# Performance work log

Hardware: AMD Instinct MI355X
Metric: run time of the kernel (lower is better)

The kernel has to match this reference:

```python
import jax, jax.numpy as jnp
import numpy as np

N_NODES = 50000
N_EDGES = 800000
IN_DIM = 128
OUT_DIM = 64
BN_EPS = 1e-5
LRELU_SLOPE = 0.01


def setup_inputs() -> dict:
    key = jax.random.key(0)
    ks = jax.random.split(key, 8)
    feature = jax.random.normal(ks[0], (N_NODES, IN_DIM), dtype=jnp.float32)
    src = jax.random.randint(ks[1], (N_EDGES,), 0, N_NODES)
    dst = jax.random.randint(ks[2], (N_EDGES,), 0, N_NODES)
    edge_weight = jax.random.uniform(ks[3], (N_EDGES,), dtype=jnp.float32)
    # learned params
    b1 = jnp.zeros((IN_DIM,), jnp.float32)                      # gcn1 bias (weight=False)
    gamma1 = jnp.ones((IN_DIM,), jnp.float32)
    beta1 = jnp.zeros((IN_DIM,), jnp.float32)
    W2 = jax.random.normal(ks[4], (IN_DIM, OUT_DIM), jnp.float32) * (2.0 / IN_DIM) ** 0.5  # kaiming-ish
    b2 = jnp.zeros((OUT_DIM,), jnp.float32)
    gamma2 = jnp.ones((OUT_DIM,), jnp.float32)
    beta2 = jnp.zeros((OUT_DIM,), jnp.float32)
    return dict(feature=feature, edge_weight=edge_weight, b1=b1, gamma1=gamma1,
                beta1=beta1, W2=W2, b2=b2, gamma2=gamma2, beta2=beta2,
                src=src, dst=dst)


def _degrees(src, dst, n):
    ones = jnp.ones(src.shape[0], jnp.float32)
    deg_out = jnp.clip(jax.ops.segment_sum(ones, src, num_segments=n), 1.0)
    deg_in = jnp.clip(jax.ops.segment_sum(ones, dst, num_segments=n), 1.0)
    return deg_out, deg_in


def _graph_conv(x, src, dst, edge_w, W, b, deg_out, deg_in):
    # DGL GraphConv, norm='both': D_in^{-1/2} * A(_w) * D_out^{-1/2} * x (@ W) + b
    h = x * jax.lax.rsqrt(deg_out)[:, None]
    if W is not None:
        h = h @ W  # [N, out]
    m = h[src]                                   # gather  [E, d]
    if edge_w is not None:
        m = m * edge_w[:, None]
    agg = jax.ops.segment_sum(m, dst, num_segments=x.shape[0])  # scatter-add [N, d]
    return agg * jax.lax.rsqrt(deg_in)[:, None] + b


def _batchnorm(x, gamma, beta):
    mean = jnp.mean(x, axis=0)
    var = jnp.var(x, axis=0)  # biased, as torch BN training-mode normalization
    return gamma * (x - mean) * jax.lax.rsqrt(var + BN_EPS) + beta


def reference(feature, edge_weight, b1, gamma1, beta1, W2, b2, gamma2, beta2, src, dst):
    deg_out, deg_in = _degrees(src, dst, feature.shape[0])
    h = _graph_conv(feature, src, dst, edge_weight, None, b1, deg_out, deg_in)
    h = _batchnorm(h, gamma1, beta1)              # dropout = identity (eval)
    h1 = jnp.where(h > 0, h, LRELU_SLOPE * h)     # LeakyReLU
    h2 = _graph_conv(h1, src, dst, None, W2, b2, deg_out, deg_in)
    h = _batchnorm(h2, gamma2, beta2)
    return jax.nn.softmax(h, axis=-1)
```

## Files before the change

### kernel.cpp

```cpp
#include <hip/hip_runtime.h>
#include <cstddef>

typedef unsigned int u32;

#define N_NODES 50000
#define N_EDGES 800000
#define D1 128
#define D2 64
#define BN_EPS 1e-5f
#define LRELU 0.01f
#define ELLW 64
#define C1B 2048
#define C2B 2048

__device__ __forceinline__ u32 f2bf(float x) {
    u32 u = __float_as_uint(x);
    return (u + 0x7fffu + ((u >> 16) & 1u)) >> 16;
}

__global__ void k_build(const int* __restrict__ src, const int* __restrict__ dst,
                        const float* __restrict__ ew, const float* __restrict__ feature,
                        int* __restrict__ cnt_in, int* __restrict__ cnt_out,
                        u32* __restrict__ ell, u32* __restrict__ feat_bf) {
    const int e = blockIdx.x * 256 + threadIdx.x;
    if (e < N_EDGES) {
        int d = dst[e];
        int slot = atomicAdd(&cnt_in[d], 1);
        if (slot < ELLW)
            ell[(size_t)d * ELLW + slot] = ((u32)src[e] << 16) | f2bf(ew[e]);
        atomicAdd(&cnt_out[src[e]], 1);
    }
    const int TOTU = N_NODES * (D1 / 2);
    for (int i = e; i < TOTU; i += N_EDGES) {
        float2 v = *(const float2*)&feature[2 * (size_t)i];
        feat_bf[i] = f2bf(v.x) | (f2bf(v.y) << 16);
    }
}

__global__ __launch_bounds__(128) void k_conv1(const u32* __restrict__ feat_bf,
                                               const int* __restrict__ cnt_in,
                                               const int* __restrict__ cnt_out,
                                               const u32* __restrict__ ell,
                                               const float* __restrict__ b1,
                                               float* __restrict__ t1,
                                               float* __restrict__ part1) {
    const int w = threadIdx.x >> 6, lane = threadIdx.x & 63;
    __shared__ int   s_idx[2][ELLW];
    __shared__ float s_sc[2][ELLW];
    __shared__ float red[2][D1];
    const float bb0 = b1[2 * lane], bb1 = b1[2 * lane + 1];
    float s0 = 0.f, q0 = 0.f, s1 = 0.f, q1 = 0.f;
    for (int base = blockIdx.x * 2; base < N_NODES; base += 2 * C1B) {
        const int node = base + w;
        const int cnt = cnt_in[node];
        const int deg = min(cnt, ELLW);
        if (lane < deg) {
            u32 ent = ell[(size_t)node * ELLW + lane];
            int s = ent >> 16;
            s_idx[w][lane] = s;
            s_sc[w][lane]  = __uint_as_float(ent << 16) * rsqrtf((float)max(cnt_out[s], 1));
        }
        __syncthreads();
        float a0 = 0.f, a1 = 0.f;
        for (int j = 0; j < deg; ++j) {
            u32 p = feat_bf[(size_t)s_idx[w][j] * (D1 / 2) + lane];
            float sc = s_sc[w][j];
            a0 += __uint_as_float(p << 16) * sc;
            a1 += __uint_as_float(p & 0xffff0000u) * sc;
        }
        float r = rsqrtf((float)max(cnt, 1));
        float v0 = a0 * r + bb0, v1 = a1 * r + bb1;
        float2 v = {v0, v1};
        *(float2*)&t1[(size_t)node * D1 + 2 * lane] = v;
        s0 += v0; q0 += v0 * v0; s1 += v1; q1 += v1 * v1;
        __syncthreads();
    }
    red[w][2 * lane] = s0; red[w][2 * lane + 1] = s1;
    __syncthreads();
    if (w == 0) {
        part1[(size_t)blockIdx.x * 2 * D1 + 2 * lane]     = red[0][2 * lane] + red[1][2 * lane];
        part1[(size_t)blockIdx.x * 2 * D1 + 2 * lane + 1] = red[0][2 * lane + 1] + red[1][2 * lane + 1];
    }
    __syncthreads();
    red[w][2 * lane] = q0; red[w][2 * lane + 1] = q1;
    __syncthreads();
    if (w == 0) {
        part1[(size_t)blockIdx.x * 2 * D1 + D1 + 2 * lane]     = red[0][2 * lane] + red[1][2 * lane];
        part1[(size_t)blockIdx.x * 2 * D1 + D1 + 2 * lane + 1] = red[0][2 * lane + 1] + red[1][2 * lane + 1];
    }
}

template <int D>
__global__ __launch_bounds__(128) void k_bn_final(const float* __restrict__ part, int nblk,
                                                  const float* __restrict__ gamma,
                                                  const float* __restrict__ beta,
                                                  float* __restrict__ coef) {
    const int c = blockIdx.x;
    const int t = threadIdx.x;
    __shared__ float sh[4];
    float s = 0.f, q = 0.f;
    for (int b = t; b < nblk; b += 128) {
        s += part[(size_t)b * 2 * D + c];
        q += part[(size_t)b * 2 * D + D + c];
    }
    for (int o = 32; o >= 1; o >>= 1) {
        s += __shfl_xor(s, o, 64);
        q += __shfl_xor(q, o, 64);
    }
    if ((t & 63) == 0) { sh[(t >> 6) * 2] = s; sh[(t >> 6) * 2 + 1] = q; }
    __syncthreads();
    if (t == 0) {
        s = sh[0] + sh[2];
        q = sh[1] + sh[3];
        const float inv_n = 1.f / (float)N_NODES;
        float mean = s * inv_n;
        float var  = q * inv_n - mean * mean;
        float rstd = rsqrtf(var + BN_EPS);
        float a = gamma[c] * rstd;
        coef[c]     = a;
        coef[D + c] = beta[c] - mean * a;
    }
}

__global__ __launch_bounds__(256) void k_mm(const float* __restrict__ t1,
                                            const float* __restrict__ coef1,
                                            const int* __restrict__ cnt_out,
                                            const float* __restrict__ W2,
                                            u32* __restrict__ g_bf) {
    __shared__ float sW[D1 * D2];
    __shared__ float sX[32][132];
    const int tid = threadIdx.x;
    const int r0 = blockIdx.x * 32;
    for (int i = tid; i < D1 * D2 / 4; i += 256)
        ((float4*)sW)[i] = ((const float4*)W2)[i];
    for (int i = tid; i < 32 * (D1 / 4); i += 256) {
        int r = i >> 5, k4 = i & 31;
        int row = r0 + r;
        float4 v = {0.f, 0.f, 0.f, 0.f};
        if (row < N_NODES) {
            v = *(const float4*)&t1[(size_t)row * D1 + 4 * k4];
            float ro = rsqrtf((float)max(cnt_out[row], 1));
            int k = 4 * k4;
            float x;
            x = coef1[k]     * v.x + coef1[D1 + k];     v.x = ((x > 0.f) ? x : LRELU * x) * ro;
            x = coef1[k + 1] * v.y + coef1[D1 + k + 1]; v.y = ((x > 0.f) ? x : LRELU * x) * ro;
            x = coef1[k + 2] * v.z + coef1[D1 + k + 2]; v.z = ((x > 0.f) ? x : LRELU * x) * ro;
            x = coef1[k + 3] * v.w + coef1[D1 + k + 3]; v.w = ((x > 0.f) ? x : LRELU * x) * ro;
        }
        *(float4*)&sX[r][4 * k4] = v;
    }
    __syncthreads();
    const int c  = tid & 63;
    const int rg = tid >> 6;
    float acc[8] = {0.f, 0.f, 0.f, 0.f, 0.f, 0.f, 0.f, 0.f};
    for (int k = 0; k < D1; k += 4) {
        float w0 = sW[k * D2 + c];
        float w1 = sW[(k + 1) * D2 + c];
        float w2 = sW[(k + 2) * D2 + c];
        float w3 = sW[(k + 3) * D2 + c];
#pragma unroll
        for (int j = 0; j < 8; ++j) {
            float4 x4 = *(const float4*)&sX[rg + 4 * j][k];
            acc[j] = fmaf(x4.x, w0, acc[j]);
            acc[j] = fmaf(x4.y, w1, acc[j]);
            acc[j] = fmaf(x4.z, w2, acc[j]);
            acc[j] = fmaf(x4.w, w3, acc[j]);
        }
    }
#pragma unroll
    for (int j = 0; j < 8; ++j) {
        int row = r0 + rg + 4 * j;
        float partner = __shfl_xor(acc[j], 1, 64);
        if (row < N_NODES && (c & 1) == 0)
            g_bf[(size_t)row * (D2 / 2) + (c >> 1)] = f2bf(acc[j]) | (f2bf(partner) << 16);
    }
}

__global__ __launch_bounds__(128) void k_conv2(const u32* __restrict__ g_bf,
                                               const int* __restrict__ cnt_in,
                                               const u32* __restrict__ ell,
                                               const float* __restrict__ b2,
                                               float* __restrict__ out,
                                               float* __restrict__ part2) {
    const int w = threadIdx.x >> 6, lane = threadIdx.x & 63;
    const int m = lane & 31, half = lane >> 5;
    __shared__ int   s_idx[2][ELLW];
    __shared__ float red[2][D2];
    const float bb0 = b2[2 * m], bb1 = b2[2 * m + 1];
    float s0 = 0.f, q0 = 0.f, s1 = 0.f, q1 = 0.f;
    for (int base = blockIdx.x * 2; base < N_NODES; base += 2 * C2B) {
        const int node = base + w;
        const int cnt = cnt_in[node];
        const int deg = min(cnt, ELLW);
        if (lane < deg) s_idx[w][lane] = ell[(size_t)node * ELLW + lane] >> 16;
        __syncthreads();
        float a0 = 0.f, a1 = 0.f;
        for (int j = half; j < deg; j += 2) {
            u32 p = g_bf[(size_t)s_idx[w][j] * (D2 / 2) + m];
            a0 += __uint_as_float(p << 16);
            a1 += __uint_as_float(p & 0xffff0000u);
        }
        a0 += __shfl_xor(a0, 32, 64);
        a1 += __shfl_xor(a1, 32, 64);
        float r = rsqrtf((float)max(cnt, 1));
        float v0 = a0 * r + bb0, v1 = a1 * r + bb1;
        if (half == 0) {
            float2 v = {v0, v1};
            *(float2*)&out[(size_t)node * D2 + 2 * m] = v;
            s0 += v0; q0 += v0 * v0; s1 += v1; q1 += v1 * v1;
        }
        __syncthreads();
    }
    if (half == 0) { red[w][2 * m] = s0; red[w][2 * m + 1] = s1; }
    __syncthreads();
    if (w == 0 && half == 0) {
        part2[(size_t)blockIdx.x * 2 * D2 + 2 * m]     = red[0][2 * m] + red[1][2 * m];
        part2[(size_t)blockIdx.x * 2 * D2 + 2 * m + 1] = red[0][2 * m + 1] + red[1][2 * m + 1];
    }
    __syncthreads();
    if (half == 0) { red[w][2 * m] = q0; red[w][2 * m + 1] = q1; }
    __syncthreads();
    if (w == 0 && half == 0) {
        part2[(size_t)blockIdx.x * 2 * D2 + D2 + 2 * m]     = red[0][2 * m] + red[1][2 * m];
        part2[(size_t)blockIdx.x * 2 * D2 + D2 + 2 * m + 1] = red[0][2 * m + 1] + red[1][2 * m + 1];
    }
}

__global__ __launch_bounds__(256) void k_softmax(float* __restrict__ out,
                                                 const float* __restrict__ coef2) {
    const int tid = threadIdx.x;
    const int lane = tid & 63;
    const int row = blockIdx.x * 4 + (tid >> 6);
    if (row >= N_NODES) return;
    float v = out[(size_t)row * D2 + lane] * coef2[lane] + coef2[D2 + lane];
    float m = v;
    for (int o = 32; o >= 1; o >>= 1) m = fmaxf(m, __shfl_xor(m, o, 64));
    float e = expf(v - m);
    float s = e;
    for (int o = 32; o >= 1; o >>= 1) s += __shfl_xor(s, o, 64);
    out[(size_t)row * D2 + lane] = e / s;
}

extern "C" void kernel_launch(void* const* d_in, const int* in_sizes, int n_in,
                              void* d_out, int out_size, void* d_ws, size_t ws_size,
                              hipStream_t stream) {
    const float* feature = (const float*)d_in[0];
    const float* edge_w  = (const float*)d_in[1];
    const float* b1      = (const float*)d_in[2];
    const float* gamma1  = (const float*)d_in[3];
    const float* beta1   = (const float*)d_in[4];
    const float* W2      = (const float*)d_in[5];
    const float* b2      = (const float*)d_in[6];
    const float* gamma2  = (const float*)d_in[7];
    const float* beta2   = (const float*)d_in[8];
    const int*   src     = (const int*)d_in[9];
    const int*   dst     = (const int*)d_in[10];

    float* out = (float*)d_out;

    int*   cnt_in  = (int*)d_ws;
    int*   cnt_out = cnt_in + 50000;
    float* coef1   = (float*)(cnt_out + 50000);
    float* coef2   = coef1 + 256;
    u32*   ell     = (u32*)(coef2 + 128);
    float* t1      = (float*)(ell + (size_t)N_NODES * ELLW);
    u32*   feat_bf = (u32*)(t1 + (size_t)N_NODES * D1);
    u32*   g_bf    = feat_bf + (size_t)N_NODES * (D1 / 2);
    float* part1   = (float*)g_bf;
    float* part2   = t1;

    hipMemsetAsync(cnt_in, 0, 2 * 50000 * sizeof(int), stream);

    const int EB = (N_EDGES + 255) / 256;
    k_build<<<EB, 256, 0, stream>>>(src, dst, edge_w, feature,
                                    cnt_in, cnt_out, ell, feat_bf);

    k_conv1<<<C1B, 128, 0, stream>>>(feat_bf, cnt_in, cnt_out, ell, b1, t1, part1);
    k_bn_final<D1><<<D1, 128, 0, stream>>>(part1, C1B, gamma1, beta1, coef1);

    k_mm<<<(N_NODES + 31) / 32, 256, 0, stream>>>(t1, coef1, cnt_out, W2, g_bf);

    k_conv2<<<C2B, 128, 0, stream>>>(g_bf, cnt_in, ell, b2, out, part2);
    k_bn_final<D2><<<D2, 128, 0, stream>>>(part2, C2B, gamma2, beta2, coef2);

    k_softmax<<<(N_NODES + 3) / 4, 256, 0, stream>>>(out, coef2);
}
```

Measured before the change: 236.0 us.

## Split degree counters into four sub-queues and store conv1 output in bf16

Spreads the build-phase atomic counters over four replicated count arrays chosen by edge index, so contention on hot destination and source nodes is reduced. Each node's ELL row becomes four fixed sub-slots, and the conv kernels rebuild a packed neighbour list from prefix offsets. A new small kernel precomputes the in and out inverse square-root degrees, so the conv and matmul kernels no longer recompute them per edge. The intermediate conv1 output is now stored as bf16, halving its write and read traffic, at the cost of lower precision before batchnorm and matmul. The ELL row also grows from 64 to 96 slots, adding memory footprint, and any sub-queue holding more than 24 edges drops the extra ones.

```diff
diff --git a/kernel.cpp b/kernel.cpp
--- a/kernel.cpp
+++ b/kernel.cpp
@@ -5,11 +5,13 @@
 
 #define N_NODES 50000
 #define N_EDGES 800000
+#define NPAD 50016
 #define D1 128
 #define D2 64
 #define BN_EPS 1e-5f
 #define LRELU 0.01f
-#define ELLW 64
+#define ELLW 96
+#define QCAP 24
 #define C1B 2048
 #define C2B 2048
 
@@ -25,10 +27,11 @@
     const int e = blockIdx.x * 256 + threadIdx.x;
     if (e < N_EDGES) {
         int d = dst[e];
-        int slot = atomicAdd(&cnt_in[d], 1);
-        if (slot < ELLW)
-            ell[(size_t)d * ELLW + slot] = ((u32)src[e] << 16) | f2bf(ew[e]);
-        atomicAdd(&cnt_out[src[e]], 1);
+        int r = e & 3;
+        int slot = atomicAdd(&cnt_in[r * NPAD + d], 1);
+        if (slot < QCAP)
+            ell[(size_t)d * ELLW + r * QCAP + slot] = ((u32)src[e] << 16) | f2bf(ew[e]);
+        atomicAdd(&cnt_out[r * NPAD + src[e]], 1);
     }
     const int TOTU = N_NODES * (D1 / 2);
     for (int i = e; i < TOTU; i += N_EDGES) {
@@ -37,12 +40,28 @@
     }
 }
 
+__global__ __launch_bounds__(256) void k_rs(const int* __restrict__ cnt_in,
+                                            const int* __restrict__ cnt_out,
+                                            int4* __restrict__ qcnt,
+                                            float* __restrict__ rs_in,
+                                            float* __restrict__ rs_out) {
+    int i = blockIdx.x * 256 + threadIdx.x;
+    if (i < N_NODES) {
+        int c0 = cnt_in[i], c1 = cnt_in[NPAD + i], c2 = cnt_in[2 * NPAD + i], c3 = cnt_in[3 * NPAD + i];
+        rs_in[i] = rsqrtf((float)max(c0 + c1 + c2 + c3, 1));
+        qcnt[i] = make_int4(min(c0, QCAP), min(c1, QCAP), min(c2, QCAP), min(c3, QCAP));
+        int o = cnt_out[i] + cnt_out[NPAD + i] + cnt_out[2 * NPAD + i] + cnt_out[3 * NPAD + i];
+        rs_out[i] = rsqrtf((float)max(o, 1));
+    }
+}
+
 __global__ __launch_bounds__(128) void k_conv1(const u32* __restrict__ feat_bf,
-                                               const int* __restrict__ cnt_in,
-                                               const int* __restrict__ cnt_out,
+                                               const int4* __restrict__ qcnt,
+                                               const float* __restrict__ rs_in,
+                                               const float* __restrict__ rs_out,
                                                const u32* __restrict__ ell,
                                                const float* __restrict__ b1,
-                                               float* __restrict__ t1,
+                                               u32* __restrict__ t1_bf,
                                                float* __restrict__ part1) {
     const int w = threadIdx.x >> 6, lane = threadIdx.x & 63;
     __shared__ int   s_idx[2][ELLW];
@@ -52,13 +71,15 @@
     float s0 = 0.f, q0 = 0.f, s1 = 0.f, q1 = 0.f;
     for (int base = blockIdx.x * 2; base < N_NODES; base += 2 * C1B) {
         const int node = base + w;
-        const int cnt = cnt_in[node];
-        const int deg = min(cnt, ELLW);
-        if (lane < deg) {
-            u32 ent = ell[(size_t)node * ELLW + lane];
+        const int4 qc = qcnt[node];
+        const int p1 = qc.x, p2 = p1 + qc.y, p3 = p2 + qc.z, deg = p3 + qc.w;
+        for (int l = lane; l < deg; l += 64) {
+            int r3 = (l >= p1) + (l >= p2) + (l >= p3);
+            int br = (r3 == 0) ? 0 : (r3 == 1) ? p1 : (r3 == 2) ? p2 : p3;
+            u32 ent = ell[(size_t)node * ELLW + r3 * QCAP + (l - br)];
             int s = ent >> 16;
-            s_idx[w][lane] = s;
-            s_sc[w][lane]  = __uint_as_float(ent << 16) * rsqrtf((float)max(cnt_out[s], 1));
+            s_idx[w][l] = s;
+            s_sc[w][l]  = __uint_as_float(ent << 16) * rs_out[s];
         }
         __syncthreads();
         float a0 = 0.f, a1 = 0.f;
@@ -68,10 +89,9 @@
             a0 += __uint_as_float(p << 16) * sc;
             a1 += __uint_as_float(p & 0xffff0000u) * sc;
         }
-        float r = rsqrtf((float)max(cnt, 1));
+        float r = rs_in[node];
         float v0 = a0 * r + bb0, v1 = a1 * r + bb1;
-        float2 v = {v0, v1};
-        *(float2*)&t1[(size_t)node * D1 + 2 * lane] = v;
+        t1_bf[(size_t)node * (D1 / 2) + lane] = f2bf(v0) | (f2bf(v1) << 16);
         s0 += v0; q0 += v0 * v0; s1 += v1; q1 += v1 * v1;
         __syncthreads();
     }
@@ -122,9 +142,9 @@
     }
 }
 
-__global__ __launch_bounds__(256) void k_mm(const float* __restrict__ t1,
+__global__ __launch_bounds__(256) void k_mm(const u32* __restrict__ t1_bf,
                                             const float* __restrict__ coef1,
-                                            const int* __restrict__ cnt_out,
+                                            const float* __restrict__ rs_out,
                                             const float* __restrict__ W2,
                                             u32* __restrict__ g_bf) {
     __shared__ float sW[D1 * D2];
@@ -133,21 +153,20 @@
     const int r0 = blockIdx.x * 32;
     for (int i = tid; i < D1 * D2 / 4; i += 256)
         ((float4*)sW)[i] = ((const float4*)W2)[i];
-    for (int i = tid; i < 32 * (D1 / 4); i += 256) {
-        int r = i >> 5, k4 = i & 31;
+    for (int i = tid; i < 32 * (D1 / 2); i += 256) {
+        int r = i >> 6, k2 = i & 63;
         int row = r0 + r;
-        float4 v = {0.f, 0.f, 0.f, 0.f};
+        float vx = 0.f, vy = 0.f;
         if (row < N_NODES) {
-            v = *(const float4*)&t1[(size_t)row * D1 + 4 * k4];
-            float ro = rsqrtf((float)max(cnt_out[row], 1));
-            int k = 4 * k4;
+            u32 p = t1_bf[(size_t)row * (D1 / 2) + k2];
+            float ro = rs_out[row];
+            int k = 2 * k2;
             float x;
-            x = coef1[k]     * v.x + coef1[D1 + k];     v.x = ((x > 0.f) ? x : LRELU * x) * ro;
-            x = coef1[k + 1] * v.y + coef1[D1 + k + 1]; v.y = ((x > 0.f) ? x : LRELU * x) * ro;
-            x = coef1[k + 2] * v.z + coef1[D1 + k + 2]; v.z = ((x > 0.f) ? x : LRELU * x) * ro;
-            x = coef1[k + 3] * v.w + coef1[D1 + k + 3]; v.w = ((x > 0.f) ? x : LRELU * x) * ro;
-        }
-        *(float4*)&sX[r][4 * k4] = v;
+            x = coef1[k]     * __uint_as_float(p << 16)         + coef1[D1 + k];     vx = ((x > 0.f) ? x : LRELU * x) * ro;
+            x = coef1[k + 1] * __uint_as_float(p & 0xffff0000u) + coef1[D1 + k + 1]; vy = ((x > 0.f) ? x : LRELU * x) * ro;
+        }
+        sX[r][2 * k2] = vx;
+        sX[r][2 * k2 + 1] = vy;
     }
     __syncthreads();
     const int c  = tid & 63;
@@ -177,7 +196,8 @@
 }
 
 __global__ __launch_bounds__(128) void k_conv2(const u32* __restrict__ g_bf,
-                                               const int* __restrict__ cnt_in,
+                                               const int4* __restrict__ qcnt,
+                                               const float* __restrict__ rs_in,
                                                const u32* __restrict__ ell,
                                                const float* __restrict__ b2,
                                                float* __restrict__ out,
@@ -190,9 +210,13 @@
     float s0 = 0.f, q0 = 0.f, s1 = 0.f, q1 = 0.f;
     for (int base = blockIdx.x * 2; base < N_NODES; base += 2 * C2B) {
         const int node = base + w;
-        const int cnt = cnt_in[node];
-        const int deg = min(cnt, ELLW);
-        if (lane < deg) s_idx[w][lane] = ell[(size_t)node * ELLW + lane] >> 16;
+        const int4 qc = qcnt[node];
+        const int p1 = qc.x, p2 = p1 + qc.y, p3 = p2 + qc.z, deg = p3 + qc.w;
+        for (int l = lane; l < deg; l += 64) {
+            int r3 = (l >= p1) + (l >= p2) + (l >= p3);
+            int br = (r3 == 0) ? 0 : (r3 == 1) ? p1 : (r3 == 2) ? p2 : p3;
+            s_idx[w][l] = ell[(size_t)node * ELLW + r3 * QCAP + (l - br)] >> 16;
+        }
         __syncthreads();
         float a0 = 0.f, a1 = 0.f;
         for (int j = half; j < deg; j += 2) {
@@ -202,7 +226,7 @@
         }
         a0 += __shfl_xor(a0, 32, 64);
         a1 += __shfl_xor(a1, 32, 64);
-        float r = rsqrtf((float)max(cnt, 1));
+        float r = rs_in[node];
         float v0 = a0 * r + bb0, v1 = a1 * r + bb1;
         if (half == 0) {
             float2 v = {v0, v1};
@@ -259,28 +283,32 @@
     float* out = (float*)d_out;
 
     int*   cnt_in  = (int*)d_ws;
-    int*   cnt_out = cnt_in + 50000;
-    float* coef1   = (float*)(cnt_out + 50000);
+    int*   cnt_out = cnt_in + 4 * NPAD;
+    int4*  qcnt    = (int4*)(cnt_out + 4 * NPAD);
+    float* rs_in   = (float*)((int*)qcnt + 200000);
+    float* rs_out  = rs_in + 50000;
+    float* coef1   = rs_out + 50000;
     float* coef2   = coef1 + 256;
-    u32*   ell     = (u32*)(coef2 + 128);
-    float* t1      = (float*)(ell + (size_t)N_NODES * ELLW);
-    u32*   feat_bf = (u32*)(t1 + (size_t)N_NODES * D1);
-    u32*   g_bf    = feat_bf + (size_t)N_NODES * (D1 / 2);
-    float* part1   = (float*)g_bf;
-    float* part2   = t1;
-
-    hipMemsetAsync(cnt_in, 0, 2 * 50000 * sizeof(int), stream);
+    float* part1   = coef2 + 128;
+    u32*   ell     = (u32*)(part1 + 524288);
+    u32*   t1_bf   = ell + (size_t)N_NODES * ELLW;
+    u32*   feat_bf = t1_bf + (size_t)N_NODES * (D1 / 2);
+    u32*   g_bf    = feat_bf;
+    float* part2   = part1;
+
+    hipMemsetAsync(cnt_in, 0, 8 * NPAD * sizeof(int), stream);
 
     const int EB = (N_EDGES + 255) / 256;
     k_build<<<EB, 256, 0, stream>>>(src, dst, edge_w, feature,
                                     cnt_in, cnt_out, ell, feat_bf);
-
-    k_conv1<<<C1B, 128, 0, stream>>>(feat_bf, cnt_in, cnt_out, ell, b1, t1, part1);
+    k_rs<<<(N_NODES + 255) / 256, 256, 0, stream>>>(cnt_in, cnt_out, qcnt, rs_in, rs_out);
+
+    k_conv1<<<C1B, 128, 0, stream>>>(feat_bf, qcnt, rs_in, rs_out, ell, b1, t1_bf, part1);
     k_bn_final<D1><<<D1, 128, 0, stream>>>(part1, C1B, gamma1, beta1, coef1);
 
-    k_mm<<<(N_NODES + 31) / 32, 256, 0, stream>>>(t1, coef1, cnt_out, W2, g_bf);
-
-    k_conv2<<<C2B, 128, 0, stream>>>(g_bf, cnt_in, ell, b2, out, part2);
+    k_mm<<<(N_NODES + 31) / 32, 256, 0, stream>>>(t1_bf, coef1, rs_out, W2, g_bf);
+
+    k_conv2<<<C2B, 128, 0, stream>>>(g_bf, qcnt, rs_in, ell, b2, out, part2);
     k_bn_final<D2><<<D2, 128, 0, stream>>>(part2, C2B, gamma2, beta2, coef2);
 
     k_softmax<<<(N_NODES + 3) / 4, 256, 0, stream>>>(out, coef2);
```

Measured after the change: 250.0 us. 5.9% more time.

## Store conv1 output as bf16 and split conv1 gather across half-waves

Applied to the files above, without the earlier changes.

The first graph convolution now writes its intermediate result as packed bf16 instead of fp32, which halves the write traffic and the matrix-multiply kernel's read traffic. Its gather loop now uses two half-waves that each take alternate neighbours with 8-byte loads, combined with a shuffle. The workspace layout is reorganised so the partial BN sums get their own region and g_bf reuses the feat_bf buffer. The cost is extra rounding of the intermediate before batch norm and the matmul, and only half the lanes doing the epilogue.

```diff
diff --git a/kernel.cpp b/kernel.cpp
--- a/kernel.cpp
+++ b/kernel.cpp
@@ -17,6 +17,8 @@
     u32 u = __float_as_uint(x);
     return (u + 0x7fffu + ((u >> 16) & 1u)) >> 16;
 }
+__device__ __forceinline__ float bflo(u32 p) { return __uint_as_float(p << 16); }
+__device__ __forceinline__ float bfhi(u32 p) { return __uint_as_float(p & 0xffff0000u); }
 
 __global__ void k_build(const int* __restrict__ src, const int* __restrict__ dst,
                         const float* __restrict__ ew, const float* __restrict__ feature,
@@ -42,14 +44,16 @@
                                                const int* __restrict__ cnt_out,
                                                const u32* __restrict__ ell,
                                                const float* __restrict__ b1,
-                                               float* __restrict__ t1,
+                                               u32* __restrict__ t1_bf,
                                                float* __restrict__ part1) {
     const int w = threadIdx.x >> 6, lane = threadIdx.x & 63;
+    const int m = lane & 31, half = lane >> 5;
     __shared__ int   s_idx[2][ELLW];
     __shared__ float s_sc[2][ELLW];
     __shared__ float red[2][D1];
-    const float bb0 = b1[2 * lane], bb1 = b1[2 * lane + 1];
-    float s0 = 0.f, q0 = 0.f, s1 = 0.f, q1 = 0.f;
+    const float bb0 = b1[4 * m], bb1 = b1[4 * m + 1], bb2 = b1[4 * m + 2], bb3 = b1[4 * m + 3];
+    float s0 = 0.f, s1 = 0.f, s2 = 0.f, s3 = 0.f;
+    float q0 = 0.f, q1 = 0.f, q2 = 0.f, q3 = 0.f;
     for (int base = blockIdx.x * 2; base < N_NODES; base += 2 * C1B) {
         const int node = base + w;
         const int cnt = cnt_in[node];
@@ -58,35 +62,51 @@
             u32 ent = ell[(size_t)node * ELLW + lane];
             int s = ent >> 16;
             s_idx[w][lane] = s;
-            s_sc[w][lane]  = __uint_as_float(ent << 16) * rsqrtf((float)max(cnt_out[s], 1));
+            s_sc[w][lane]  = bflo(ent) * rsqrtf((float)max(cnt_out[s], 1));
         }
         __syncthreads();
-        float a0 = 0.f, a1 = 0.f;
-        for (int j = 0; j < deg; ++j) {
-            u32 p = feat_bf[(size_t)s_idx[w][j] * (D1 / 2) + lane];
+        float a0 = 0.f, a1 = 0.f, a2 = 0.f, a3 = 0.f;
+        for (int j = half; j < deg; j += 2) {
+            uint2 p = *(const uint2*)&feat_bf[(size_t)s_idx[w][j] * (D1 / 2) + 2 * m];
             float sc = s_sc[w][j];
-            a0 += __uint_as_float(p << 16) * sc;
-            a1 += __uint_as_float(p & 0xffff0000u) * sc;
-        }
-        float r = rsqrtf((float)max(cnt, 1));
-        float v0 = a0 * r + bb0, v1 = a1 * r + bb1;
-        float2 v = {v0, v1};
-        *(float2*)&t1[(size_t)node * D1 + 2 * lane] = v;
-        s0 += v0; q0 += v0 * v0; s1 += v1; q1 += v1 * v1;
+            a0 += bflo(p.x) * sc; a1 += bfhi(p.x) * sc;
+            a2 += bflo(p.y) * sc; a3 += bfhi(p.y) * sc;
+        }
+        a0 += __shfl_xor(a0, 32, 64); a1 += __shfl_xor(a1, 32, 64);
+        a2 += __shfl_xor(a2, 32, 64); a3 += __shfl_xor(a3, 32, 64);
+        if (half == 0) {
+            float r = rsqrtf((float)max(cnt, 1));
+            float v0 = a0 * r + bb0, v1 = a1 * r + bb1;
+            float v2 = a2 * r + bb2, v3 = a3 * r + bb3;
+            uint2 o;
+            o.x = f2bf(v0) | (f2bf(v1) << 16);
+            o.y = f2bf(v2) | (f2bf(v3) << 16);
+            *(uint2*)&t1_bf[(size_t)node * (D1 / 2) + 2 * m] = o;
+            s0 += v0; q0 += v0 * v0; s1 += v1; q1 += v1 * v1;
+            s2 += v2; q2 += v2 * v2; s3 += v3; q3 += v3 * v3;
+        }
         __syncthreads();
     }
-    red[w][2 * lane] = s0; red[w][2 * lane + 1] = s1;
-    __syncthreads();
-    if (w == 0) {
-        part1[(size_t)blockIdx.x * 2 * D1 + 2 * lane]     = red[0][2 * lane] + red[1][2 * lane];
-        part1[(size_t)blockIdx.x * 2 * D1 + 2 * lane + 1] = red[0][2 * lane + 1] + red[1][2 * lane + 1];
-    }
-    __syncthreads();
-    red[w][2 * lane] = q0; red[w][2 * lane + 1] = q1;
-    __syncthreads();
-    if (w == 0) {
-        part1[(size_t)blockIdx.x * 2 * D1 + D1 + 2 * lane]     = red[0][2 * lane] + red[1][2 * lane];
-        part1[(size_t)blockIdx.x * 2 * D1 + D1 + 2 * lane + 1] = red[0][2 * lane + 1] + red[1][2 * lane + 1];
+    if (half == 0) {
+        red[w][4 * m] = s0; red[w][4 * m + 1] = s1;
+        red[w][4 * m + 2] = s2; red[w][4 * m + 3] = s3;
+    }
+    __syncthreads();
+    if (w == 0 && half == 0) {
+#pragma unroll
+        for (int k = 0; k < 4; ++k)
+            part1[(size_t)blockIdx.x * 2 * D1 + 4 * m + k] = red[0][4 * m + k] + red[1][4 * m + k];
+    }
+    __syncthreads();
+    if (half == 0) {
+        red[w][4 * m] = q0; red[w][4 * m + 1] = q1;
+        red[w][4 * m + 2] = q2; red[w][4 * m + 3] = q3;
+    }
+    __syncthreads();
+    if (w == 0 && half == 0) {
+#pragma unroll
+        for (int k = 0; k < 4; ++k)
+            part1[(size_t)blockIdx.x * 2 * D1 + D1 + 4 * m + k] = red[0][4 * m + k] + red[1][4 * m + k];
     }
 }
 
@@ -122,7 +142,7 @@
     }
 }
 
-__global__ __launch_bounds__(256) void k_mm(const float* __restrict__ t1,
+__global__ __launch_bounds__(256) void k_mm(const u32* __restrict__ t1_bf,
                                             const float* __restrict__ coef1,
                                             const int* __restrict__ cnt_out,
                                             const float* __restrict__ W2,
@@ -133,21 +153,20 @@
     const int r0 = blockIdx.x * 32;
     for (int i = tid; i < D1 * D2 / 4; i += 256)
         ((float4*)sW)[i] = ((const float4*)W2)[i];
-    for (int i = tid; i < 32 * (D1 / 4); i += 256) {
-        int r = i >> 5, k4 = i & 31;
+    for (int i = tid; i < 32 * (D1 / 2); i += 256) {
+        int r = i >> 6, k2 = i & 63;
         int row = r0 + r;
-        float4 v = {0.f, 0.f, 0.f, 0.f};
+        float vx = 0.f, vy = 0.f;
         if (row < N_NODES) {
-            v = *(const float4*)&t1[(size_t)row * D1 + 4 * k4];
+            u32 p = t1_bf[(size_t)row * (D1 / 2) + k2];
             float ro = rsqrtf((float)max(cnt_out[row], 1));
-            int k = 4 * k4;
+            int k = 2 * k2;
             float x;
-            x = coef1[k]     * v.x + coef1[D1 + k];     v.x = ((x > 0.f) ? x : LRELU * x) * ro;
-            x = coef1[k + 1] * v.y + coef1[D1 + k + 1]; v.y = ((x > 0.f) ? x : LRELU * x) * ro;
-            x = coef1[k + 2] * v.z + coef1[D1 + k + 2]; v.z = ((x > 0.f) ? x : LRELU * x) * ro;
-            x = coef1[k + 3] * v.w + coef1[D1 + k + 3]; v.w = ((x > 0.f) ? x : LRELU * x) * ro;
-        }
-        *(float4*)&sX[r][4 * k4] = v;
+            x = coef1[k]     * bflo(p) + coef1[D1 + k];     vx = ((x > 0.f) ? x : LRELU * x) * ro;
+            x = coef1[k + 1] * bfhi(p) + coef1[D1 + k + 1]; vy = ((x > 0.f) ? x : LRELU * x) * ro;
+        }
+        sX[r][2 * k2] = vx;
+        sX[r][2 * k2 + 1] = vy;
     }
     __syncthreads();
     const int c  = tid & 63;
@@ -197,8 +216,8 @@
         float a0 = 0.f, a1 = 0.f;
         for (int j = half; j < deg; j += 2) {
             u32 p = g_bf[(size_t)s_idx[w][j] * (D2 / 2) + m];
-            a0 += __uint_as_float(p << 16);
-            a1 += __uint_as_float(p & 0xffff0000u);
+            a0 += bflo(p);
+            a1 += bfhi(p);
         }
         a0 += __shfl_xor(a0, 32, 64);
         a1 += __shfl_xor(a1, 32, 64);
@@ -262,12 +281,12 @@
     int*   cnt_out = cnt_in + 50000;
     float* coef1   = (float*)(cnt_out + 50000);
     float* coef2   = coef1 + 256;
-    u32*   ell     = (u32*)(coef2 + 128);
-    float* t1      = (float*)(ell + (size_t)N_NODES * ELLW);
-    u32*   feat_bf = (u32*)(t1 + (size_t)N_NODES * D1);
-    u32*   g_bf    = feat_bf + (size_t)N_NODES * (D1 / 2);
-    float* part1   = (float*)g_bf;
-    float* part2   = t1;
+    float* part1   = coef2 + 128;
+    u32*   ell     = (u32*)(part1 + 524288);
+    u32*   t1_bf   = ell + (size_t)N_NODES * ELLW;
+    u32*   feat_bf = t1_bf + (size_t)N_NODES * (D1 / 2);
+    u32*   g_bf    = feat_bf;
+    float* part2   = part1;
 
     hipMemsetAsync(cnt_in, 0, 2 * 50000 * sizeof(int), stream);
 
@@ -275,10 +294,10 @@
     k_build<<<EB, 256, 0, stream>>>(src, dst, edge_w, feature,
                                     cnt_in, cnt_out, ell, feat_bf);
 
-    k_conv1<<<C1B, 128, 0, stream>>>(feat_bf, cnt_in, cnt_out, ell, b1, t1, part1);
+    k_conv1<<<C1B, 128, 0, stream>>>(feat_bf, cnt_in, cnt_out, ell, b1, t1_bf, part1);
     k_bn_final<D1><<<D1, 128, 0, stream>>>(part1, C1B, gamma1, beta1, coef1);
 
-    k_mm<<<(N_NODES + 31) / 32, 256, 0, stream>>>(t1, coef1, cnt_out, W2, g_bf);
+    k_mm<<<(N_NODES + 31) / 32, 256, 0, stream>>>(t1_bf, coef1, cnt_out, W2, g_bf);
 
     k_conv2<<<C2B, 128, 0, stream>>>(g_bf, cnt_in, ell, b2, out, part2);
     k_bn_final<D2><<<D2, 128, 0, stream>>>(part2, C2B, gamma2, beta2, coef2);
```

Result: slower. 254.7 us (+7.9%).
